# Kernel tuning notes

Measured on AMD Instinct MI355X. Metric: run time of the kernel, lower is better.

Reference implementation:

```python
import jax, jax.numpy as jnp
import numpy as np
from jax import lax

N = 4194304  # batch of FP16 values, each encoded as 16 spike bits

# MSB-first bit weights / shift amounts for the [S,E4..E0,M9..M0] layout
_POW = np.array([1 << (15 - i) for i in range(16)], dtype=np.int32)
_SHIFTS = np.array([15 - i for i in range(16)], dtype=np.int32)


def _pack(bits):
    """[..., 16] {0,1} float bits (MSB first) -> float16 scalar per row."""
    b = jnp.round(bits).astype(jnp.int32)
    u = jnp.sum(b * _POW, axis=-1).astype(jnp.uint16)
    return lax.bitcast_convert_type(u, jnp.float16)


def _unpack(f):
    """float16 [...] -> [..., 16] {0,1} float32 bits (MSB first)."""
    u = lax.bitcast_convert_type(f, jnp.uint16).astype(jnp.int32)
    return ((u[..., None] >> _SHIFTS) & 1).astype(jnp.float32)


def _sample_bits(key, n):
    bits = jax.random.bernoulli(key, 0.5, (n, 16)).astype(jnp.float32)
    # avoid exponent == 31 (Inf/NaN encodings) so outputs are well-defined finite fp16
    all_ones = jnp.prod(bits[:, 1:6], axis=-1, keepdims=True)
    return bits.at[:, 5:6].set(bits[:, 5:6] * (1.0 - all_ones))


def setup_inputs() -> dict:
    key = jax.random.key(0)
    ka, kb = jax.random.split(key)
    return {"A": _sample_bits(ka, N), "B": _sample_bits(kb, N)}


def reference(A, B):
    # The SNN gate network implements an IEEE-754 FP16 adder (round-to-nearest-even,
    # subnormal support, overflow/underflow handling) over bit-encoded operands.
    # fp16 add computed via fp32 is bit-exact here (24 >= 2*11+2, Figueroa's theorem),
    # which is what XLA does for float16 on CPU.
    s = _pack(A) + _pack(B)
    return _unpack(s)
```

## Files before the change

kernel.cpp:

```cpp
#include <hip/hip_runtime.h>
#include <hip/hip_fp16.h>


__global__ __launch_bounds__(256) void spike_fp16_add_kernel(
    const float4* __restrict__ A, const float4* __restrict__ B,
    float4* __restrict__ O, int nrows)
{
    int i = blockIdx.x * blockDim.x + threadIdx.x;
    if (i >= nrows) return;

    const size_t base = (size_t)i * 4;

    float4 a0 = A[base + 0], a1 = A[base + 1], a2 = A[base + 2], a3 = A[base + 3];
    float4 b0 = B[base + 0], b1 = B[base + 1], b2 = B[base + 2], b3 = B[base + 3];

    uint32_t ua =
        ((uint32_t)a0.x << 15) | ((uint32_t)a0.y << 14) | ((uint32_t)a0.z << 13) | ((uint32_t)a0.w << 12) |
        ((uint32_t)a1.x << 11) | ((uint32_t)a1.y << 10) | ((uint32_t)a1.z <<  9) | ((uint32_t)a1.w <<  8) |
        ((uint32_t)a2.x <<  7) | ((uint32_t)a2.y <<  6) | ((uint32_t)a2.z <<  5) | ((uint32_t)a2.w <<  4) |
        ((uint32_t)a3.x <<  3) | ((uint32_t)a3.y <<  2) | ((uint32_t)a3.z <<  1) | ((uint32_t)a3.w);
    uint32_t ub =
        ((uint32_t)b0.x << 15) | ((uint32_t)b0.y << 14) | ((uint32_t)b0.z << 13) | ((uint32_t)b0.w << 12) |
        ((uint32_t)b1.x << 11) | ((uint32_t)b1.y << 10) | ((uint32_t)b1.z <<  9) | ((uint32_t)b1.w <<  8) |
        ((uint32_t)b2.x <<  7) | ((uint32_t)b2.y <<  6) | ((uint32_t)b2.z <<  5) | ((uint32_t)b2.w <<  4) |
        ((uint32_t)b3.x <<  3) | ((uint32_t)b3.y <<  2) | ((uint32_t)b3.z <<  1) | ((uint32_t)b3.w);

    float fa = __half2float(__ushort_as_half((unsigned short)ua));
    float fb = __half2float(__ushort_as_half((unsigned short)ub));
    uint32_t us = (uint32_t)__half_as_ushort(__float2half_rn(fa + fb));

    float4 o0, o1, o2, o3;
    o0.x = (float)((us >> 15) & 1u); o0.y = (float)((us >> 14) & 1u);
    o0.z = (float)((us >> 13) & 1u); o0.w = (float)((us >> 12) & 1u);
    o1.x = (float)((us >> 11) & 1u); o1.y = (float)((us >> 10) & 1u);
    o1.z = (float)((us >>  9) & 1u); o1.w = (float)((us >>  8) & 1u);
    o2.x = (float)((us >>  7) & 1u); o2.y = (float)((us >>  6) & 1u);
    o2.z = (float)((us >>  5) & 1u); o2.w = (float)((us >>  4) & 1u);
    o3.x = (float)((us >>  3) & 1u); o3.y = (float)((us >>  2) & 1u);
    o3.z = (float)((us >>  1) & 1u); o3.w = (float)( us         & 1u);

    O[base + 0] = o0;
    O[base + 1] = o1;
    O[base + 2] = o2;
    O[base + 3] = o3;
}

extern "C" void kernel_launch(void* const* d_in, const int* in_sizes, int n_in,
                              void* d_out, int out_size, void* d_ws, size_t ws_size,
                              hipStream_t stream) {
    const float4* A = (const float4*)d_in[0];
    const float4* B = (const float4*)d_in[1];
    float4* O = (float4*)d_out;

    int nrows = in_sizes[0] / 16;
    int block = 256;
    int grid = (nrows + block - 1) / block;
    spike_fp16_add_kernel<<<grid, block, 0, stream>>>(A, B, O, nrows);
}
```

Before: 585.9 us.

## Coalesce loads by spreading each row across four lanes with shuffles

Each row's four float4 chunks are now handled by four adjacent lanes, so consecutive lanes touch consecutive float4s and global loads and stores coalesce fully. Each lane packs a 4-bit nibble and combines it with the others through xor shuffles, then every lane computes the same fp16 add and writes only its own nibble. The previous layout had each thread read a 64-byte stride, so a wave's accesses were spread out. This adds cross-lane shuffles and redundant fp16 arithmetic in every lane, and the early return inside the loop could leave shuffle partners missing when the tail is partial.

```diff
diff --git a/kernel.cpp b/kernel.cpp
--- a/kernel.cpp
+++ b/kernel.cpp
@@ -4,45 +4,47 @@
 
 __global__ __launch_bounds__(256) void spike_fp16_add_kernel(
     const float4* __restrict__ A, const float4* __restrict__ B,
-    float4* __restrict__ O, int nrows)
+    float4* __restrict__ O, int nf4)
 {
-    int i = blockIdx.x * blockDim.x + threadIdx.x;
-    if (i >= nrows) return;
+    const int lane = threadIdx.x & 63;
+    const int waveBase = ((blockIdx.x * blockDim.x + threadIdx.x) >> 6) * 256;
+    const int q = lane & 3;
+    const int sh = 12 - 4 * q;
 
-    const size_t base = (size_t)i * 4;
+    #pragma unroll
+    for (int k = 0; k < 4; ++k) {
+        const int f4 = waveBase + k * 64 + lane;
+        if (f4 >= nf4) return;
 
-    float4 a0 = A[base + 0], a1 = A[base + 1], a2 = A[base + 2], a3 = A[base + 3];
-    float4 b0 = B[base + 0], b1 = B[base + 1], b2 = B[base + 2], b3 = B[base + 3];
+        float4 a = A[f4];
+        float4 b = B[f4];
 
-    uint32_t ua =
-        ((uint32_t)a0.x << 15) | ((uint32_t)a0.y << 14) | ((uint32_t)a0.z << 13) | ((uint32_t)a0.w << 12) |
-        ((uint32_t)a1.x << 11) | ((uint32_t)a1.y << 10) | ((uint32_t)a1.z <<  9) | ((uint32_t)a1.w <<  8) |
-        ((uint32_t)a2.x <<  7) | ((uint32_t)a2.y <<  6) | ((uint32_t)a2.z <<  5) | ((uint32_t)a2.w <<  4) |
-        ((uint32_t)a3.x <<  3) | ((uint32_t)a3.y <<  2) | ((uint32_t)a3.z <<  1) | ((uint32_t)a3.w);
-    uint32_t ub =
-        ((uint32_t)b0.x << 15) | ((uint32_t)b0.y << 14) | ((uint32_t)b0.z << 13) | ((uint32_t)b0.w << 12) |
-        ((uint32_t)b1.x << 11) | ((uint32_t)b1.y << 10) | ((uint32_t)b1.z <<  9) | ((uint32_t)b1.w <<  8) |
-        ((uint32_t)b2.x <<  7) | ((uint32_t)b2.y <<  6) | ((uint32_t)b2.z <<  5) | ((uint32_t)b2.w <<  4) |
-        ((uint32_t)b3.x <<  3) | ((uint32_t)b3.y <<  2) | ((uint32_t)b3.z <<  1) | ((uint32_t)b3.w);
+        uint32_t na = ((uint32_t)a.x << 3) | ((uint32_t)a.y << 2) |
+                      ((uint32_t)a.z << 1) |  (uint32_t)a.w;
+        uint32_t nb = ((uint32_t)b.x << 3) | ((uint32_t)b.y << 2) |
+                      ((uint32_t)b.z << 1) |  (uint32_t)b.w;
 
-    float fa = __half2float(__ushort_as_half((unsigned short)ua));
-    float fb = __half2float(__ushort_as_half((unsigned short)ub));
-    uint32_t us = (uint32_t)__half_as_ushort(__float2half_rn(fa + fb));
+        uint32_t ua = na << sh;
+        uint32_t ub = nb << sh;
 
-    float4 o0, o1, o2, o3;
-    o0.x = (float)((us >> 15) & 1u); o0.y = (float)((us >> 14) & 1u);
-    o0.z = (float)((us >> 13) & 1u); o0.w = (float)((us >> 12) & 1u);
-    o1.x = (float)((us >> 11) & 1u); o1.y = (float)((us >> 10) & 1u);
-    o1.z = (float)((us >>  9) & 1u); o1.w = (float)((us >>  8) & 1u);
-    o2.x = (float)((us >>  7) & 1u); o2.y = (float)((us >>  6) & 1u);
-    o2.z = (float)((us >>  5) & 1u); o2.w = (float)((us >>  4) & 1u);
-    o3.x = (float)((us >>  3) & 1u); o3.y = (float)((us >>  2) & 1u);
-    o3.z = (float)((us >>  1) & 1u); o3.w = (float)( us         & 1u);
+        ua |= (uint32_t)__shfl_xor((int)ua, 1);
+        ua |= (uint32_t)__shfl_xor((int)ua, 2);
+        ub |= (uint32_t)__shfl_xor((int)ub, 1);
+        ub |= (uint32_t)__shfl_xor((int)ub, 2);
 
-    O[base + 0] = o0;
-    O[base + 1] = o1;
-    O[base + 2] = o2;
-    O[base + 3] = o3;
+        float fa = __half2float(__ushort_as_half((unsigned short)ua));
+        float fb = __half2float(__ushort_as_half((unsigned short)ub));
+        uint32_t us = (uint32_t)__half_as_ushort(__float2half_rn(fa + fb));
+
+        uint32_t ns = (us >> sh) & 0xFu;
+        float4 o;
+        o.x = (float)((ns >> 3) & 1u);
+        o.y = (float)((ns >> 2) & 1u);
+        o.z = (float)((ns >> 1) & 1u);
+        o.w = (float)( ns       & 1u);
+
+        O[f4] = o;
+    }
 }
 
 extern "C" void kernel_launch(void* const* d_in, const int* in_sizes, int n_in,
@@ -52,8 +54,9 @@
     const float4* B = (const float4*)d_in[1];
     float4* O = (float4*)d_out;
 
-    int nrows = in_sizes[0] / 16;
+    int nf4 = in_sizes[0] / 4;
     int block = 256;
-    int grid = (nrows + block - 1) / block;
-    spike_fp16_add_kernel<<<grid, block, 0, stream>>>(A, B, O, nrows);
+    int threads = nf4 / 4;
+    int grid = (threads + block - 1) / block;
+    spike_fp16_add_kernel<<<grid, block, 0, stream>>>(A, B, O, nf4);
 }
```

New measurement: 577.3 us. About the same (-1.5%).
